# Kernel optimization log

Hardware: AMD Instinct MI355X
Metric: run time of the kernel (lower is better)

The kernel has to match this reference:

```python
import jax, jax.numpy as jnp
import numpy as np
import math

D_MODEL = 1024
NUM_HEADS = 16
D_K = D_MODEL // NUM_HEADS
B, S = 2, 2048


def setup_inputs() -> dict:
    key = jax.random.key(0)
    ks = jax.random.split(key, 13)
    scale = 1.0 / math.sqrt(D_MODEL)
    inp = {
        "q": jax.random.normal(ks[0], (B, S, D_MODEL), jnp.float32),
        "k": jax.random.normal(ks[1], (B, S, D_MODEL), jnp.float32),
        "v": jax.random.normal(ks[2], (B, S, D_MODEL), jnp.float32),
        "mask": jax.random.randint(ks[3], (B, 1, S, S), 0, 2, jnp.int32),
        # torch nn.Linear params: y = x @ W.T + b
        "wQ_w": jax.random.normal(ks[4], (D_MODEL, D_MODEL), jnp.float32) * scale,
        "wQ_b": jax.random.normal(ks[5], (D_MODEL,), jnp.float32) * scale,
        "wK_w": jax.random.normal(ks[6], (D_MODEL, D_MODEL), jnp.float32) * scale,
        "wK_b": jax.random.normal(ks[7], (D_MODEL,), jnp.float32) * scale,
        "wV_w": jax.random.normal(ks[8], (D_MODEL, D_MODEL), jnp.float32) * scale,
        "wV_b": jax.random.normal(ks[9], (D_MODEL,), jnp.float32) * scale,
        "wO_w": jax.random.normal(ks[10], (D_MODEL, D_MODEL), jnp.float32) * scale,
        "wO_b": jax.random.normal(ks[11], (D_MODEL,), jnp.float32) * scale,
    }
    return inp


def _split_heads(x):
    # [B, S, D] -> [B, H, S, dK]
    b, s, _ = x.shape
    return x.reshape(b, s, NUM_HEADS, D_K).transpose(0, 2, 1, 3)


def reference(q, k, v, mask, wQ_w, wQ_b, wK_w, wK_b, wV_w, wV_b, wO_w, wO_b):
    qh = _split_heads(q @ wQ_w.T + wQ_b)
    kh = _split_heads(k @ wK_w.T + wK_b)
    vh = _split_heads(v @ wV_w.T + wV_b)
    # scores: [B, H, S, S] -- materialized as in the original module
    scores = jnp.einsum("bhsd,bhtd->bhst", qh, kh) / math.sqrt(D_K)
    scores = jnp.where(mask == 0, jnp.float32(-1e9), scores)
    attn = jax.nn.softmax(scores, axis=-1)
    out = jnp.einsum("bhst,bhtd->bhsd", attn, vh)  # [B, H, S, dK]
    out = out.transpose(0, 2, 1, 3).reshape(q.shape[0], -1, D_MODEL)
    return out @ wO_w.T + wO_b
```

## Files before the change

### kernel.cpp

```cpp
#include <hip/hip_runtime.h>
#include <hip/hip_bf16.h>
#include <stdint.h>
#include <math.h>

#define NHEADS 16
#define DK 64
#define BATCH 2
#define SEQ 2048
#define DMODEL 1024
#define MROWS (BATCH*SEQ)

typedef __bf16 bf16x8 __attribute__((ext_vector_type(8)));
typedef float  f32x4  __attribute__((ext_vector_type(4)));
typedef float  f32x16 __attribute__((ext_vector_type(16)));

typedef const __attribute__((address_space(1))) void* gas_ptr;
typedef       __attribute__((address_space(3))) void* las_ptr;

__device__ __forceinline__ void async16(const void* g, void* l) {
  __builtin_amdgcn_global_load_lds((gas_ptr)g, (las_ptr)l, 16, 0, 0);
}

__device__ __forceinline__ unsigned short f2bf_raw(float f) {
  __hip_bfloat16 h = __float2bfloat16(f);
  return *reinterpret_cast<unsigned short*>(&h);
}

__device__ __forceinline__ float fast_exp2(float x) {
#if __has_builtin(__builtin_amdgcn_exp2f)
  return __builtin_amdgcn_exp2f(x);
#else
  float r;
  asm("v_exp_f32 %0, %1\ns_nop 1" : "=v"(r) : "v"(x));
  return r;
#endif
}

__device__ __forceinline__ uint32_t pk_bf16(float lo, float hi2) {
  uint32_t r;
  asm("v_cvt_pk_bf16_f32 %0, %1, %2" : "=v"(r) : "v"(lo), "v"(hi2));
  return r;
}

__device__ __forceinline__ void half_swap(uint32_t& a, uint32_t& b) {
  auto r = __builtin_amdgcn_permlane32_swap(a, b, false, false);
  a = (uint32_t)r[0];
  b = (uint32_t)r[1];
}

__device__ __forceinline__ float mask_sel(uint32_t msel, float s, float c) {
  uint32_t su = __float_as_uint(s), cu = __float_as_uint(c);
  return __uint_as_float((msel & su) | (~msel & cu));
}

__device__ __forceinline__ f32x16 zero16() {
  f32x16 z;
#pragma unroll
  for (int i = 0; i < 16; ++i) z[i] = 0.f;
  return z;
}

__global__ void prep_kernel(const float* __restrict__ q,
                            const float* __restrict__ k,
                            const float* __restrict__ v,
                            const float* __restrict__ w0,
                            const float* __restrict__ w1,
                            const float* __restrict__ w2,
                            const float* __restrict__ w3,
                            ushort4* __restrict__ out,
                            const int* __restrict__ mask,
                            uint32_t* __restrict__ bits) {
  if (blockIdx.x < 16384) {
    int i = blockIdx.x * 256 + threadIdx.x;
    const float* src;
    int local;
    if (i < 3145728) {
      int seg = i >> 20;
      src = (seg == 0) ? q : (seg == 1) ? k : v;
      local = i & 1048575;
    } else {
      int j = i - 3145728;
      int seg = j >> 18;
      src = (seg == 0) ? w0 : (seg == 1) ? w1 : (seg == 2) ? w2 : w3;
      local = j & 262143;
    }
    float4 f = reinterpret_cast<const float4*>(src)[local];
    ushort4 u;
    u.x = f2bf_raw(f.x); u.y = f2bf_raw(f.y);
    u.z = f2bf_raw(f.z); u.w = f2bf_raw(f.w);
    out[i] = u;
  } else {
    int i = (blockIdx.x - 16384) * 256 + threadIdx.x;
    unsigned long long bal = __ballot(mask[i] != 0);
    int lane = threadIdx.x & 63;
    if (lane == 0)  bits[i >> 5] = (uint32_t)bal;
    if (lane == 32) bits[i >> 5] = (uint32_t)(bal >> 32);
  }
}


__device__ __forceinline__ void gemm_core_128(
    const __hip_bfloat16* __restrict__ A, const __hip_bfloat16* __restrict__ Bw,
    int K, int m0, int n0,
    __hip_bfloat16* sA, __hip_bfloat16* sB, f32x4 acc[4][4]) {
  const int lane = threadIdx.x & 63;
  const int wid  = threadIdx.x >> 6;
  const int wr = wid >> 1, wc = wid & 1;
  const int crow = lane >> 2;
  const int ccol = (lane & 3) * 8;

#pragma unroll
  for (int mi = 0; mi < 4; ++mi)
#pragma unroll
    for (int ni = 0; ni < 4; ++ni) acc[mi][ni] = f32x4{0.f, 0.f, 0.f, 0.f};

  for (int k0 = 0; k0 < K; k0 += 32) {
    for (int c = wid; c < 8; c += 4) {
      async16(A  + (size_t)(m0 + c * 16 + crow) * K + k0 + ccol,
              (char*)sA + c * 1024 + lane * 16);
      async16(Bw + (size_t)(n0 + c * 16 + crow) * K + k0 + ccol,
              (char*)sB + c * 1024 + lane * 16);
    }
    __syncthreads();
    bf16x8 af[4], bfr[4];
#pragma unroll
    for (int mi = 0; mi < 4; ++mi)
      af[mi] = *reinterpret_cast<const bf16x8*>(
          &sA[(wr * 64 + mi * 16 + (lane & 15)) * 32 + 8 * (lane >> 4)]);
#pragma unroll
    for (int ni = 0; ni < 4; ++ni)
      bfr[ni] = *reinterpret_cast<const bf16x8*>(
          &sB[(wc * 64 + ni * 16 + (lane & 15)) * 32 + 8 * (lane >> 4)]);
    __builtin_amdgcn_s_setprio(1);
#pragma unroll
    for (int mi = 0; mi < 4; ++mi)
#pragma unroll
      for (int ni = 0; ni < 4; ++ni)
        acc[mi][ni] = __builtin_amdgcn_mfma_f32_16x16x32_bf16(
            af[mi], bfr[ni], acc[mi][ni], 0, 0, 0);
    __builtin_amdgcn_s_setprio(0);
    __syncthreads();
  }
}

__global__ __launch_bounds__(256, 3) void qkv_gemm_kernel(
    const __hip_bfloat16* __restrict__ Xq, const __hip_bfloat16* __restrict__ Xk,
    const __hip_bfloat16* __restrict__ Xv,
    const __hip_bfloat16* __restrict__ Wq, const __hip_bfloat16* __restrict__ Wk,
    const __hip_bfloat16* __restrict__ Wv,
    const float* __restrict__ bq, const float* __restrict__ bk,
    const float* __restrict__ bv,
    __hip_bfloat16* __restrict__ Qh, __hip_bfloat16* __restrict__ Kh,
    __hip_bfloat16* __restrict__ VhT) {
  __shared__ __hip_bfloat16 sA[128 * 32];
  __shared__ __hip_bfloat16 sB[128 * 32];
  const int z = blockIdx.z;
  const __hip_bfloat16* A  = (z == 0) ? Xq : (z == 1) ? Xk : Xv;
  const __hip_bfloat16* Bw = (z == 0) ? Wq : (z == 1) ? Wk : Wv;
  const float* bias        = (z == 0) ? bq : (z == 1) ? bk : bv;
  __hip_bfloat16* Co       = (z == 0) ? Qh : (z == 1) ? Kh : VhT;
  const int m0 = blockIdx.x * 128, n0 = blockIdx.y * 128;
  f32x4 acc[4][4];
  gemm_core_128(A, Bw, DMODEL, m0, n0, sA, sB, acc);

  const int lane = threadIdx.x & 63, wid = threadIdx.x >> 6;
  const int wr = wid >> 1, wc = wid & 1;
  const int l15 = lane & 15, lg = lane >> 4;
  const float osc = (z == 0) ? 0.18033688f : 1.0f;
  if (z != 2) {
#pragma unroll
    for (int mi = 0; mi < 4; ++mi)
#pragma unroll
      for (int ni = 0; ni < 4; ++ni) {
        int j = n0 + wc * 64 + ni * 16 + l15;
        float bj = bias[j];
        int hh = j >> 6, d = j & 63;
#pragma unroll
        for (int r = 0; r < 4; ++r) {
          int i = m0 + wr * 64 + mi * 16 + lg * 4 + r;
          int bb = i >> 11, s = i & 2047;
          float v = (acc[mi][ni][r] + bj) * osc;
          Co[((size_t)(bb * NHEADS + hh) * SEQ + s) * DK + d] = __float2bfloat16(v);
        }
      }
  } else {
#pragma unroll
    for (int mi = 0; mi < 4; ++mi)
#pragma unroll
      for (int ni = 0; ni < 4; ++ni) {
        int j = n0 + wc * 64 + ni * 16 + l15;
        float bj = bias[j];
        int hh = j >> 6, d = j & 63;
        int i0 = m0 + wr * 64 + mi * 16 + lg * 4;
        int bb = i0 >> 11, sbase = i0 & 2047;
        ushort4 st;
        st.x = f2bf_raw(acc[mi][ni][0] + bj);
        st.y = f2bf_raw(acc[mi][ni][1] + bj);
        st.z = f2bf_raw(acc[mi][ni][2] + bj);
        st.w = f2bf_raw(acc[mi][ni][3] + bj);
        *reinterpret_cast<ushort4*>(
            &Co[((size_t)(bb * NHEADS + hh) * DK + d) * SEQ + sbase]) = st;
      }
  }
}

__global__ __launch_bounds__(256, 3) void out_gemm_kernel(
    const __hip_bfloat16* __restrict__ A, const __hip_bfloat16* __restrict__ Ww,
    const float* __restrict__ bias, float* __restrict__ C) {
  __shared__ __hip_bfloat16 sA[128 * 32];
  __shared__ __hip_bfloat16 sB[128 * 32];
  const int m0 = blockIdx.x * 128, n0 = blockIdx.y * 128;
  f32x4 acc[4][4];
  gemm_core_128(A, Ww, DMODEL, m0, n0, sA, sB, acc);
  const int lane = threadIdx.x & 63, wid = threadIdx.x >> 6;
  const int wr = wid >> 1, wc = wid & 1;
#pragma unroll
  for (int mi = 0; mi < 4; ++mi)
#pragma unroll
    for (int ni = 0; ni < 4; ++ni) {
      int j = n0 + wc * 64 + ni * 16 + (lane & 15);
      float bj = bias[j];
#pragma unroll
      for (int r = 0; r < 4; ++r) {
        int i = m0 + wr * 64 + mi * 16 + (lane >> 4) * 4 + r;
        C[(size_t)i * DMODEL + j] = acc[mi][ni][r] + bj;
      }
    }
}


__global__ __launch_bounds__(256, 3) void attn_kernel(
    const __hip_bfloat16* __restrict__ Qh, const __hip_bfloat16* __restrict__ Kh,
    const __hip_bfloat16* __restrict__ VhT, const uint32_t* __restrict__ mbits,
    __hip_bfloat16* __restrict__ AO) {
  __shared__ __hip_bfloat16 Ks[2][64 * 64];
  __shared__ __hip_bfloat16 Vs[2][64 * 64];
  __shared__ float sRed[4 * 32];

  const int tid = threadIdx.x, lane = tid & 63, wid = tid >> 6;
  const int l31 = lane & 31, hi = lane >> 5;
  const int sw = l31 & 7;
  const int bh = blockIdx.y, b = bh >> 4, h = bh & 15;
  const int q0g = blockIdx.x * 128 + wid * 32;

  const __hip_bfloat16* Qp = Qh  + (size_t)bh * SEQ * DK;
  const __hip_bfloat16* Kp = Kh  + (size_t)bh * SEQ * DK;
  const __hip_bfloat16* Vp = VhT + (size_t)bh * DK * SEQ;
  const uint32_t* mb = mbits + (size_t)b * SEQ * (SEQ / 32)
                             + (size_t)(q0g + l31) * (SEQ / 32);
  float* sRedW = &sRed[wid * 32];

  bf16x8 qf[4];
#pragma unroll
  for (int dc = 0; dc < 4; ++dc)
    qf[dc] = *reinterpret_cast<const bf16x8*>(
        &Qp[(size_t)(q0g + l31) * DK + dc * 16 + hi * 8]);

  f32x16 acc0 = zero16(), acc1 = zero16();
  float l_run = 0.f;

#define STAGE(kv0_, s_)                                                        \
  {                                                                            \
    _Pragma("unroll")                                                          \
    for (int u = 0; u < 2; ++u) {                                              \
      int c = tid + u * 256;                                                   \
      int row = c >> 3, ss = (c & 7) ^ (row & 7);                              \
      async16(Kp + (size_t)(kv0_ + row) * DK + ss * 8,                         \
              (char*)Ks[s_] + c * 16);                                         \
      async16(Vp + (size_t)row * SEQ + (kv0_) + ss * 8,                        \
              (char*)Vs[s_] + c * 16);                                         \
    }                                                                          \
  }

  STAGE(0, 0);
  uint2 mw = *reinterpret_cast<const uint2*>(mb);
  asm volatile("s_waitcnt vmcnt(0)" ::: "memory");
  __syncthreads();

  const int NT = SEQ / 64;
  for (int t = 0; t < NT; ++t) {
    const int cur = t & 1;
    if (t + 1 < NT) STAGE((t + 1) * 64, cur ^ 1);

    uint2 mw_next;
    if (t + 1 < NT) mw_next = *reinterpret_cast<const uint2*>(mb + (t + 1) * 2);
    uint32_t w0 = mw.x >> (4 * hi), w1 = mw.y >> (4 * hi);

    const __hip_bfloat16* ks = Ks[cur];
    const __hip_bfloat16* vs = Vs[cur];

    f32x16 s0 = zero16(), s1 = zero16();
    __builtin_amdgcn_s_setprio(1);
#pragma unroll
    for (int dc = 0; dc < 4; ++dc) {
      bf16x8 k0 = *reinterpret_cast<const bf16x8*>(
          &ks[(size_t)(l31) * 64 + (((dc * 2 + hi) ^ sw) * 8)]);
      bf16x8 k1 = *reinterpret_cast<const bf16x8*>(
          &ks[(size_t)(32 + l31) * 64 + (((dc * 2 + hi) ^ sw) * 8)]);
      s0 = __builtin_amdgcn_mfma_f32_32x32x16_bf16(k0, qf[dc], s0, 0, 0, 0);
      s1 = __builtin_amdgcn_mfma_f32_32x32x16_bf16(k1, qf[dc], s1, 0, 0, 0);
    }
    __builtin_amdgcn_s_setprio(0);

    union { uint32_t u[4]; bf16x8 v; } pc;
    {
      float p[16];
#pragma unroll
      for (int r = 0; r < 16; ++r) {
        const int sh = (r & 3) + 8 * (r >> 2);
        uint32_t msel = (uint32_t)__builtin_amdgcn_sbfe((int)w0, sh, 1);
        p[r] = fast_exp2(mask_sel(msel, s0[r], -1e9f));
        l_run += p[r];
      }
      uint32_t a0 = pk_bf16(p[0], p[1]),  a1 = pk_bf16(p[2], p[3]);
      uint32_t b0 = pk_bf16(p[4], p[5]),  b1 = pk_bf16(p[6], p[7]);
      uint32_t c0 = pk_bf16(p[8], p[9]),  c1 = pk_bf16(p[10], p[11]);
      uint32_t d0 = pk_bf16(p[12], p[13]), d1 = pk_bf16(p[14], p[15]);
      half_swap(a0, b0); half_swap(a1, b1);
      half_swap(c0, d0); half_swap(c1, d1);
      __builtin_amdgcn_s_setprio(1);
      pc.u[0] = a0; pc.u[1] = a1; pc.u[2] = b0; pc.u[3] = b1;
      {
        bf16x8 v0 = *reinterpret_cast<const bf16x8*>(
            &vs[(size_t)(l31) * 64 + (((0 + hi) ^ sw) * 8)]);
        bf16x8 v1 = *reinterpret_cast<const bf16x8*>(
            &vs[(size_t)(32 + l31) * 64 + (((0 + hi) ^ sw) * 8)]);
        acc0 = __builtin_amdgcn_mfma_f32_32x32x16_bf16(pc.v, v0, acc0, 0, 0, 0);
        acc1 = __builtin_amdgcn_mfma_f32_32x32x16_bf16(pc.v, v1, acc1, 0, 0, 0);
      }
      pc.u[0] = c0; pc.u[1] = c1; pc.u[2] = d0; pc.u[3] = d1;
      {
        bf16x8 v0 = *reinterpret_cast<const bf16x8*>(
            &vs[(size_t)(l31) * 64 + (((2 + hi) ^ sw) * 8)]);
        bf16x8 v1 = *reinterpret_cast<const bf16x8*>(
            &vs[(size_t)(32 + l31) * 64 + (((2 + hi) ^ sw) * 8)]);
        acc0 = __builtin_amdgcn_mfma_f32_32x32x16_bf16(pc.v, v0, acc0, 0, 0, 0);
        acc1 = __builtin_amdgcn_mfma_f32_32x32x16_bf16(pc.v, v1, acc1, 0, 0, 0);
      }
      __builtin_amdgcn_s_setprio(0);
    }
    {
      float p[16];
#pragma unroll
      for (int r = 0; r < 16; ++r) {
        const int sh = (r & 3) + 8 * (r >> 2);
        uint32_t msel = (uint32_t)__builtin_amdgcn_sbfe((int)w1, sh, 1);
        p[r] = fast_exp2(mask_sel(msel, s1[r], -1e9f));
        l_run += p[r];
      }
      uint32_t a0 = pk_bf16(p[0], p[1]),  a1 = pk_bf16(p[2], p[3]);
      uint32_t b0 = pk_bf16(p[4], p[5]),  b1 = pk_bf16(p[6], p[7]);
      uint32_t c0 = pk_bf16(p[8], p[9]),  c1 = pk_bf16(p[10], p[11]);
      uint32_t d0 = pk_bf16(p[12], p[13]), d1 = pk_bf16(p[14], p[15]);
      half_swap(a0, b0); half_swap(a1, b1);
      half_swap(c0, d0); half_swap(c1, d1);
      __builtin_amdgcn_s_setprio(1);
      pc.u[0] = a0; pc.u[1] = a1; pc.u[2] = b0; pc.u[3] = b1;
      {
        bf16x8 v0 = *reinterpret_cast<const bf16x8*>(
            &vs[(size_t)(l31) * 64 + (((4 + hi) ^ sw) * 8)]);
        bf16x8 v1 = *reinterpret_cast<const bf16x8*>(
            &vs[(size_t)(32 + l31) * 64 + (((4 + hi) ^ sw) * 8)]);
        acc0 = __builtin_amdgcn_mfma_f32_32x32x16_bf16(pc.v, v0, acc0, 0, 0, 0);
        acc1 = __builtin_amdgcn_mfma_f32_32x32x16_bf16(pc.v, v1, acc1, 0, 0, 0);
      }
      pc.u[0] = c0; pc.u[1] = c1; pc.u[2] = d0; pc.u[3] = d1;
      {
        bf16x8 v0 = *reinterpret_cast<const bf16x8*>(
            &vs[(size_t)(l31) * 64 + (((6 + hi) ^ sw) * 8)]);
        bf16x8 v1 = *reinterpret_cast<const bf16x8*>(
            &vs[(size_t)(32 + l31) * 64 + (((6 + hi) ^ sw) * 8)]);
        acc0 = __builtin_amdgcn_mfma_f32_32x32x16_bf16(pc.v, v0, acc0, 0, 0, 0);
        acc1 = __builtin_amdgcn_mfma_f32_32x32x16_bf16(pc.v, v1, acc1, 0, 0, 0);
      }
      __builtin_amdgcn_s_setprio(0);
    }

    mw = mw_next;
    asm volatile("s_waitcnt vmcnt(0)" ::: "memory");
    __syncthreads();
  }

  l_run += __shfl_xor(l_run, 32);
  if (hi == 0) sRedW[l31] = l_run;
  asm volatile("s_waitcnt lgkmcnt(0)" ::: "memory");
  __syncthreads();
#pragma unroll
  for (int r = 0; r < 16; ++r) {
    int cr = (r & 3) + 8 * (r >> 2) + 4 * hi;
    float linv = 1.0f / sRedW[cr];
    int qrow = q0g + cr;
    size_t base = ((size_t)b * SEQ + qrow) * DMODEL + h * 64 + l31;
    AO[base]      = __float2bfloat16(acc0[r] * linv);
    AO[base + 32] = __float2bfloat16(acc1[r] * linv);
  }
}


extern "C" void kernel_launch(void* const* d_in, const int* in_sizes, int n_in,
                              void* d_out, int out_size, void* d_ws, size_t ws_size,
                              hipStream_t stream) {
  const float* q    = (const float*)d_in[0];
  const float* k    = (const float*)d_in[1];
  const float* v    = (const float*)d_in[2];
  const int*   mask = (const int*)d_in[3];
  const float* wQ_w = (const float*)d_in[4];
  const float* wQ_b = (const float*)d_in[5];
  const float* wK_w = (const float*)d_in[6];
  const float* wK_b = (const float*)d_in[7];
  const float* wV_w = (const float*)d_in[8];
  const float* wV_b = (const float*)d_in[9];
  const float* wO_w = (const float*)d_in[10];
  const float* wO_b = (const float*)d_in[11];

  char* ws = (char*)d_ws;
  const size_t SZ_X = (size_t)MROWS * DMODEL * 2;
  const size_t SZ_W = (size_t)DMODEL * DMODEL * 2;
  __hip_bfloat16* Xq  = (__hip_bfloat16*)(ws);
  __hip_bfloat16* Xk  = (__hip_bfloat16*)(ws + SZ_X);
  __hip_bfloat16* Xv  = (__hip_bfloat16*)(ws + 2 * SZ_X);
  __hip_bfloat16* Wq  = (__hip_bfloat16*)(ws + 3 * SZ_X);
  __hip_bfloat16* Wk  = (__hip_bfloat16*)(ws + 3 * SZ_X + SZ_W);
  __hip_bfloat16* Wv  = (__hip_bfloat16*)(ws + 3 * SZ_X + 2 * SZ_W);
  __hip_bfloat16* Wo  = (__hip_bfloat16*)(ws + 3 * SZ_X + 3 * SZ_W);
  __hip_bfloat16* Qh  = (__hip_bfloat16*)(ws + 3 * SZ_X + 4 * SZ_W);
  __hip_bfloat16* Kh  = (__hip_bfloat16*)(ws + 4 * SZ_X + 4 * SZ_W);
  __hip_bfloat16* VhT = (__hip_bfloat16*)(ws + 5 * SZ_X + 4 * SZ_W);
  __hip_bfloat16* AO  = (__hip_bfloat16*)(ws + 6 * SZ_X + 4 * SZ_W);
  uint32_t*       MB  = (uint32_t*)      (ws + 7 * SZ_X + 4 * SZ_W);

  prep_kernel<<<49152, 256, 0, stream>>>(q, k, v, wQ_w, wK_w, wV_w, wO_w,
                                         (ushort4*)ws, mask, MB);

  qkv_gemm_kernel<<<dim3(MROWS / 128, DMODEL / 128, 3), 256, 0, stream>>>(
      Xq, Xk, Xv, Wq, Wk, Wv, wQ_b, wK_b, wV_b, Qh, Kh, VhT);

  attn_kernel<<<dim3(SEQ / 128, BATCH * NHEADS), 256, 0, stream>>>(
      Qh, Kh, VhT, MB, AO);

  out_gemm_kernel<<<dim3(MROWS / 128, DMODEL / 128), 256, 0, stream>>>(
      AO, Wo, wO_b, (float*)d_out);
}
```

Before: 267.3 us.

## Split attention KV range across two wave groups per block and merge

The attention kernel now launches 512 threads per block. Two groups of four waves each process half of the key/value sequence for the same 128 query rows, with separate double-buffered LDS tiles. At the end, group 1 writes its partial output accumulators and row sums to LDS, and group 0 adds them and normalises. This doubles the waves per CU for the latency-bound attention loop and halves each wave's serial loop length. In exchange it needs more LDS per block and an extra reduction through shared memory, and the tighter launch bounds may pressure registers.

```diff
diff --git a/kernel.cpp b/kernel.cpp
--- a/kernel.cpp
+++ b/kernel.cpp
@@ -229,26 +229,32 @@
 }
 
 
-__global__ __launch_bounds__(256, 3) void attn_kernel(
+__global__ __launch_bounds__(512, 4) void attn_kernel(
     const __hip_bfloat16* __restrict__ Qh, const __hip_bfloat16* __restrict__ Kh,
     const __hip_bfloat16* __restrict__ VhT, const uint32_t* __restrict__ mbits,
     __hip_bfloat16* __restrict__ AO) {
-  __shared__ __hip_bfloat16 Ks[2][64 * 64];
-  __shared__ __hip_bfloat16 Vs[2][64 * 64];
-  __shared__ float sRed[4 * 32];
+  __shared__ char pool[65536 + 512 + 512];
+  __hip_bfloat16* Kpool = (__hip_bfloat16*)pool;
+  __hip_bfloat16* Vpool = (__hip_bfloat16*)(pool + 32768);
+  float* sRed = (float*)(pool + 65536);
+  float* lC   = (float*)(pool + 65536 + 512);
+  float* accC = (float*)pool;
 
   const int tid = threadIdx.x, lane = tid & 63, wid = tid >> 6;
+  const int grp = wid >> 2, wq = wid & 3;
+  const int ltid = tid & 255;
   const int l31 = lane & 31, hi = lane >> 5;
   const int sw = l31 & 7;
   const int bh = blockIdx.y, b = bh >> 4, h = bh & 15;
-  const int q0g = blockIdx.x * 128 + wid * 32;
+  const int q0g = blockIdx.x * 128 + wq * 32;
+  const int kvbase = grp * (SEQ / 2);
 
   const __hip_bfloat16* Qp = Qh  + (size_t)bh * SEQ * DK;
   const __hip_bfloat16* Kp = Kh  + (size_t)bh * SEQ * DK;
   const __hip_bfloat16* Vp = VhT + (size_t)bh * DK * SEQ;
   const uint32_t* mb = mbits + (size_t)b * SEQ * (SEQ / 32)
-                             + (size_t)(q0g + l31) * (SEQ / 32);
-  float* sRedW = &sRed[wid * 32];
+                             + (size_t)(q0g + l31) * (SEQ / 32) + (kvbase >> 5);
+  float* sRedW = &sRed[wq * 32];
 
   bf16x8 qf[4];
 #pragma unroll
@@ -263,12 +269,12 @@
   {                                                                            \
     _Pragma("unroll")                                                          \
     for (int u = 0; u < 2; ++u) {                                              \
-      int c = tid + u * 256;                                                   \
+      int c = ltid + u * 256;                                                  \
       int row = c >> 3, ss = (c & 7) ^ (row & 7);                              \
-      async16(Kp + (size_t)(kv0_ + row) * DK + ss * 8,                         \
-              (char*)Ks[s_] + c * 16);                                         \
-      async16(Vp + (size_t)row * SEQ + (kv0_) + ss * 8,                        \
-              (char*)Vs[s_] + c * 16);                                         \
+      async16(Kp + (size_t)(kvbase + (kv0_) + row) * DK + ss * 8,              \
+              (char*)(Kpool + (grp * 2 + (s_)) * 4096) + c * 16);              \
+      async16(Vp + (size_t)row * SEQ + kvbase + (kv0_) + ss * 8,               \
+              (char*)(Vpool + (grp * 2 + (s_)) * 4096) + c * 16);              \
     }                                                                          \
   }
 
@@ -277,7 +283,7 @@
   asm volatile("s_waitcnt vmcnt(0)" ::: "memory");
   __syncthreads();
 
-  const int NT = SEQ / 64;
+  const int NT = SEQ / 2 / 64;
   for (int t = 0; t < NT; ++t) {
     const int cur = t & 1;
     if (t + 1 < NT) STAGE((t + 1) * 64, cur ^ 1);
@@ -286,8 +292,8 @@
     if (t + 1 < NT) mw_next = *reinterpret_cast<const uint2*>(mb + (t + 1) * 2);
     uint32_t w0 = mw.x >> (4 * hi), w1 = mw.y >> (4 * hi);
 
-    const __hip_bfloat16* ks = Ks[cur];
-    const __hip_bfloat16* vs = Vs[cur];
+    const __hip_bfloat16* ks = Kpool + (grp * 2 + cur) * 4096;
+    const __hip_bfloat16* vs = Vpool + (grp * 2 + cur) * 4096;
 
     f32x16 s0 = zero16(), s1 = zero16();
     __builtin_amdgcn_s_setprio(1);
@@ -382,17 +388,31 @@
   }
 
   l_run += __shfl_xor(l_run, 32);
-  if (hi == 0) sRedW[l31] = l_run;
-  asm volatile("s_waitcnt lgkmcnt(0)" ::: "memory");
+
+  if (grp == 1) {
+    float* myacc = &accC[(wq * 64 + lane) * 32];
+#pragma unroll
+    for (int r = 0; r < 16; ++r) { myacc[r] = acc0[r]; myacc[16 + r] = acc1[r]; }
+    if (hi == 0) lC[wq * 32 + l31] = l_run;
+  }
   __syncthreads();
-#pragma unroll
-  for (int r = 0; r < 16; ++r) {
-    int cr = (r & 3) + 8 * (r >> 2) + 4 * hi;
-    float linv = 1.0f / sRedW[cr];
-    int qrow = q0g + cr;
-    size_t base = ((size_t)b * SEQ + qrow) * DMODEL + h * 64 + l31;
-    AO[base]      = __float2bfloat16(acc0[r] * linv);
-    AO[base + 32] = __float2bfloat16(acc1[r] * linv);
+
+  if (grp == 0) {
+    const float* oacc = &accC[(wq * 64 + lane) * 32];
+#pragma unroll
+    for (int r = 0; r < 16; ++r) { acc0[r] += oacc[r]; acc1[r] += oacc[16 + r]; }
+    float l_tot = l_run + lC[wq * 32 + l31];
+    if (hi == 0) sRedW[l31] = l_tot;
+    asm volatile("s_waitcnt lgkmcnt(0)" ::: "memory");
+#pragma unroll
+    for (int r = 0; r < 16; ++r) {
+      int cr = (r & 3) + 8 * (r >> 2) + 4 * hi;
+      float linv = 1.0f / sRedW[cr];
+      int qrow = q0g + cr;
+      size_t base = ((size_t)b * SEQ + qrow) * DMODEL + h * 64 + l31;
+      AO[base]      = __float2bfloat16(acc0[r] * linv);
+      AO[base + 32] = __float2bfloat16(acc1[r] * linv);
+    }
   }
 }
 
@@ -435,7 +455,7 @@
   qkv_gemm_kernel<<<dim3(MROWS / 128, DMODEL / 128, 3), 256, 0, stream>>>(
       Xq, Xk, Xv, Wq, Wk, Wv, wQ_b, wK_b, wV_b, Qh, Kh, VhT);
 
-  attn_kernel<<<dim3(SEQ / 128, BATCH * NHEADS), 256, 0, stream>>>(
+  attn_kernel<<<dim3(SEQ / 128, BATCH * NHEADS), 512, 0, stream>>>(
       Qh, Kh, VhT, MB, AO);
 
   out_gemm_kernel<<<dim3(MROWS / 128, DMODEL / 128), 256, 0, stream>>>(
```

Result: no change. 266.6 us (-0.3%).
